# Optimization experiments

Hardware: AMD Instinct MI355X
Metric: run time of the kernel (lower is better)

Reference implementation:

```python
import jax, jax.numpy as jnp
import numpy as np

B, C, T, DIN, DOUT = 8, 8, 256, 1536, 512
RADIUS = int(round(0.05 * T))  # radius = round(0.05 * Nframe)
NEG_INF = float(jnp.finfo(jnp.float32).min)


def _suppress_1d(scores):
    # Greedy temporal NMS along T for a single cine. scores: [T]
    order = jnp.argsort(-scores)  # descending
    pos = jnp.arange(T)

    def step(carry, i):
        mask, s = carry
        keep = mask[i]
        window = (jnp.abs(pos - i) <= RADIUS) & (pos != i)
        mask = jnp.where(keep, mask & ~window, mask)
        s = jnp.where(keep, s, s.at[i].set(NEG_INF))
        return (mask, s), None

    (_, s), _ = jax.lax.scan(step, (jnp.ones(T, dtype=bool), scores), order)
    return s


def _top_p_mask(scores, p):
    # scores: [B, Tflat] non-negative; returns float {0,1} mask (detached).
    s = jax.lax.stop_gradient(scores)
    s = jnp.maximum(jnp.where(jnp.isfinite(s), s, 0.0), 0.0)
    sorted_idx = jnp.argsort(-s, axis=-1)
    sorted_s = jnp.take_along_axis(s, sorted_idx, axis=-1)
    norm = sorted_s / (sorted_s.sum(axis=-1, keepdims=True) + 1e-8)
    cum = jnp.cumsum(norm, axis=-1)
    keep = cum <= p
    keep = keep.at[..., :3].set(True)  # always keep top-3
    b_idx = jnp.arange(s.shape[0])[:, None]
    mask = jnp.zeros_like(s, dtype=bool).at[b_idx, sorted_idx].set(keep)
    return mask.astype(scores.dtype)


def setup_inputs() -> dict:
    key = jax.random.key(0)
    ks = jax.random.split(key, 6)
    return {
        "query": jax.random.normal(ks[0], (B, C, T, DIN), dtype=jnp.float32),
        "values": jax.random.normal(ks[1], (B, C, T, DIN), dtype=jnp.float32),
        "W1_w": jax.random.normal(ks[2], (DIN, DOUT), dtype=jnp.float32) / np.sqrt(DIN),
        "W1_b": jax.random.normal(ks[3], (DOUT,), dtype=jnp.float32) * 0.01,
        "V_w": jax.random.normal(ks[4], (DOUT, 1), dtype=jnp.float32) / np.sqrt(DOUT),
        "V_b": jax.random.normal(ks[5], (1,), dtype=jnp.float32) * 0.01,
    }


def reference(query, values, W1_w, W1_b, V_w, V_b):
    # raw_before_suppression = V(tanh(W1(query)))  -> [B, C, T, 1]
    h = jnp.tanh(jnp.einsum('bctd,de->bcte', query, W1_w) + W1_b)
    raw_before = jnp.einsum('bcte,eo->bcto', h, V_w) + V_b

    # greedy temporal suppression, vmapped over B*C cines
    flat = raw_before[..., 0].reshape(B * C, T)
    raw = jax.vmap(_suppress_1d)(flat).reshape(B, C, T, 1)

    score = jax.nn.sigmoid(raw)
    Tflat = C * T
    flat_probs = score[..., 0].reshape(B, Tflat)
    flat_probs = jnp.where(jnp.isfinite(flat_probs), flat_probs, 0.0)

    # eval path: top_p = 0.7 nucleus mask (detached)
    mask = _top_p_mask(flat_probs, 0.7)
    mask = (mask > 0).astype(flat_probs.dtype)

    masked_score = (flat_probs * mask).reshape(B, C, T, 1)
    sum_score = jnp.sum(masked_score, axis=(1, 2), keepdims=True)
    attn = masked_score / (sum_score + 1e-8)
    attn = jnp.where(sum_score <= 0, jnp.full_like(attn, 1.0 / Tflat), attn)

    context = jnp.sum(attn * values, axis=(1, 2))  # [B, DIN]
    return context, attn, masked_score
```

## Files before the change

kernel.cpp:

```cpp
#include <hip/hip_runtime.h>
#include <math.h>
#include <stdint.h>

#define TM 16384
#define NN 512
#define KDIM 1536
#define BM 128
#define BN 128
#define BKS 32
#define NKT 48

typedef _Float16 f16x8 __attribute__((ext_vector_type(8)));
typedef float f32x4 __attribute__((ext_vector_type(4)));

__device__ __forceinline__ unsigned short f16bits(_Float16 h) {
  union { _Float16 h; unsigned short u; } cv; cv.h = h; return cv.u;
}

__device__ __forceinline__ int swz_chunk(int row, int chunk) {
  return chunk ^ ((row >> 1) & 3);
}

__device__ __forceinline__ void gload_lds16(const void* g, void* l) {
  __builtin_amdgcn_global_load_lds(
      (const __attribute__((address_space(1))) unsigned int*)g,
      (__attribute__((address_space(3))) unsigned int*)l, 16, 0, 0);
}

__global__ __launch_bounds__(256) void convert_w1_kernel(
    const float* __restrict__ W1,
    unsigned short* __restrict__ W1ws)
{
  const int kt = blockIdx.x;
  const int nb = blockIdx.y;
  const int tid = threadIdx.x;
  const int k0 = kt * BKS, n0 = nb * BN;
  const size_t tbase = ((size_t)(nb * NKT + kt) * 2) * 4096;
#pragma unroll
  for (int i = 0; i < 16; ++i) {
    int idx = tid + i * 256;
    int nn = idx & 127, kk = idx >> 7;
    float f = W1[(size_t)(k0 + kk) * NN + n0 + nn];
    _Float16 h = (_Float16)f;
    _Float16 l = (_Float16)((f - (float)h) * 2048.0f);
    int off16 = nn * 32 + (swz_chunk(nn, kk >> 3) << 3) + (kk & 7);
    W1ws[tbase + off16] = f16bits(h);
    W1ws[tbase + 4096 + off16] = f16bits(l);
  }
}

__global__ __launch_bounds__(256, 2) void gemm_score_kernel(
    const float* __restrict__ query,
    const unsigned short* __restrict__ W1ws,
    const float* __restrict__ W1b,
    const float* __restrict__ Vw,
    float* __restrict__ raw_part)
{
  __shared__ __align__(16) char ldsb[2][32768];
  __shared__ float red[2][BM];

  const int tid = threadIdx.x;
  const int lane = tid & 63;
  const int w = tid >> 6;
  const int wr = w >> 1, wc = w & 1;
  const int lrow = lane & 15;
  const int lseg = lane >> 4;

  const int bid = blockIdx.x;
  const int lin = (bid & 7) * 64 + (bid >> 3);
  const int mb = lin >> 2, nb = lin & 3;
  const int m0 = mb * BM, n0 = nb * BN;

  f32x4 zero = {0.f, 0.f, 0.f, 0.f};
  f32x4 acc[4][4];
  f32x4 acc2[4][4];
#pragma unroll
  for (int m = 0; m < 4; ++m)
#pragma unroll
    for (int n = 0; n < 4; ++n) { acc[m][n] = zero; acc2[m][n] = zero; }

  const char* wbase = (const char*)W1ws;

  auto STAGE = [&](int kt, int bufi) {
    char* base = &ldsb[bufi][0];
    const int k0 = kt * BKS;
#pragma unroll
    for (int j = 0; j < 4; ++j) {
      int chunk = (w * 4 + j) * 64 + lane;
      int row = chunk >> 3, cp = chunk & 7;
      int kc = cp ^ (row & 7);
      gload_lds16(query + (size_t)(m0 + row) * KDIM + k0 + kc * 4,
                  base + (w * 4 + j) * 1024);
    }
    const char* tb = wbase + ((size_t)(nb * NKT + kt) * 2) * 8192;
#pragma unroll
    for (int j = 0; j < 2; ++j) {
      int off = w * 2048 + j * 1024;
      gload_lds16(tb + off + lane * 16, base + 16384 + off);
      gload_lds16(tb + 8192 + off + lane * 16, base + 24576 + off);
    }
  };

  STAGE(0, 0);
  for (int kt = 0; kt < NKT; ++kt) {
    const int cur = kt & 1;
    if (kt + 1 < NKT) {
      STAGE(kt + 1, cur ^ 1);
      asm volatile("s_waitcnt vmcnt(8)" ::: "memory");
    } else {
      asm volatile("s_waitcnt vmcnt(0)" ::: "memory");
    }
    __builtin_amdgcn_s_barrier();

    const char* base = &ldsb[cur][0];
    f16x8 afh[4], afl[4], bfh[4], bfl[4];
#pragma unroll
    for (int m = 0; m < 4; ++m) {
      int row = wr * 64 + m * 16 + lrow;
      int c0 = (lseg * 2) ^ (row & 7);
      int c1 = (lseg * 2 + 1) ^ (row & 7);
      f32x4 va = *reinterpret_cast<const f32x4*>(base + row * 128 + c0 * 16);
      f32x4 vb = *reinterpret_cast<const f32x4*>(base + row * 128 + c1 * 16);
      f16x8 h, l;
#pragma unroll
      for (int e = 0; e < 4; ++e) {
        _Float16 hh = (_Float16)va[e];
        h[e] = hh;
        l[e] = (_Float16)((va[e] - (float)hh) * 2048.0f);
      }
#pragma unroll
      for (int e = 0; e < 4; ++e) {
        _Float16 hh = (_Float16)vb[e];
        h[4 + e] = hh;
        l[4 + e] = (_Float16)((vb[e] - (float)hh) * 2048.0f);
      }
      afh[m] = h;
      afl[m] = l;
    }
#pragma unroll
    for (int n = 0; n < 4; ++n) {
      int row = wc * 64 + n * 16 + lrow;
      int off = row * 64 + (swz_chunk(row, lseg) << 4);
      bfh[n] = *reinterpret_cast<const f16x8*>(base + 16384 + off);
      bfl[n] = *reinterpret_cast<const f16x8*>(base + 24576 + off);
    }
#pragma unroll
    for (int m = 0; m < 4; ++m)
#pragma unroll
      for (int n = 0; n < 4; ++n) {
        acc[m][n]  = __builtin_amdgcn_mfma_f32_16x16x32_f16(afh[m], bfh[n], acc[m][n], 0, 0, 0);
        acc2[m][n] = __builtin_amdgcn_mfma_f32_16x16x32_f16(afh[m], bfl[n], acc2[m][n], 0, 0, 0);
        acc2[m][n] = __builtin_amdgcn_mfma_f32_16x16x32_f16(afl[m], bfh[n], acc2[m][n], 0, 0, 0);
      }
    asm volatile("s_waitcnt lgkmcnt(0)" ::: "memory");
    __builtin_amdgcn_s_barrier();
  }

  float part[4][4];
#pragma unroll
  for (int m = 0; m < 4; ++m)
#pragma unroll
    for (int r = 0; r < 4; ++r) part[m][r] = 0.f;
#pragma unroll
  for (int n = 0; n < 4; ++n) {
    int col = n0 + wc * 64 + n * 16 + lrow;
    float bias = W1b[col];
    float vw = Vw[col];
#pragma unroll
    for (int m = 0; m < 4; ++m)
#pragma unroll
      for (int r = 0; r < 4; ++r) {
        float z = acc[m][n][r] + acc2[m][n][r] * 4.8828125e-4f + bias;
        part[m][r] += tanhf(z) * vw;
      }
  }
#pragma unroll
  for (int off = 1; off < 16; off <<= 1)
#pragma unroll
    for (int m = 0; m < 4; ++m)
#pragma unroll
      for (int r = 0; r < 4; ++r)
        part[m][r] += __shfl_xor(part[m][r], off, 64);
  if (lrow == 0) {
#pragma unroll
    for (int m = 0; m < 4; ++m)
#pragma unroll
      for (int r = 0; r < 4; ++r)
        red[wc][wr * 64 + m * 16 + (lane >> 4) * 4 + r] = part[m][r];
  }
  __syncthreads();
  if (tid < BM)
    raw_part[(size_t)nb * TM + m0 + tid] = red[0][tid] + red[1][tid];
}

__global__ __launch_bounds__(64) void nms_kernel(
    const float* __restrict__ raw_part,
    const float* __restrict__ Vb,
    float* __restrict__ probs)
{
  const int cine = blockIdx.x;
  const int lane = threadIdx.x;
  __shared__ float s[256];
  __shared__ int order[256];
  float sv[4];
  const float vb = Vb[0];
#pragma unroll
  for (int q = 0; q < 4; ++q) {
    int p = q * 64 + lane;
    int idx = cine * 256 + p;
    float r = vb;
#pragma unroll
    for (int sl = 0; sl < 4; ++sl) r += raw_part[sl * TM + idx];
    sv[q] = r;
    s[p] = r;
  }
  __syncthreads();
#pragma unroll
  for (int q = 0; q < 4; ++q) {
    int p = q * 64 + lane;
    float st = sv[q];
    int rk = 0;
    for (int j = 0; j < 256; ++j) {
      float sj = s[j];
      rk += (sj > st) || (sj == st && j < p);
    }
    order[rk] = p;
  }
  __syncthreads();
  unsigned m = 0xFu;
  for (int r = 0; r < 256; ++r) {
    int i = order[r];
    int qi = i >> 6, li = i & 63;
    unsigned long long ball = __ballot((lane == li) && ((m >> qi) & 1u));
    if (ball) {
#pragma unroll
      for (int q = 0; q < 4; ++q) {
        int d = q * 64 + lane - i;
        if (d != 0 && d <= 13 && d >= -13) m &= ~(1u << q);
      }
    } else if (lane == li) {
      s[i] = -3.402823466385289e+38f;
    }
  }
  __syncthreads();
#pragma unroll
  for (int q = 0; q < 4; ++q) {
    int p = q * 64 + lane;
    probs[cine * 256 + p] = 1.0f / (1.0f + expf(-s[p]));
  }
}

__global__ __launch_bounds__(256) void topp_kernel(
    const float* __restrict__ probs,
    float* __restrict__ out)
{
  const int b = blockIdx.x;
  const int tid = threadIdx.x;
  __shared__ float p[2048];
  __shared__ int cnz[2048];
  __shared__ float sv[2048];
  __shared__ int sidx[2048];
  __shared__ unsigned char msk[2048];
  __shared__ float red[256];
  __shared__ int nnz_s;

  if (tid == 0) nnz_s = 0;
  for (int i = tid; i < 2048; i += 256) {
    p[i] = probs[b * 2048 + i];
    msk[i] = 0;
  }
  __syncthreads();
  float lsum = 0.f;
  for (int i = tid; i < 2048; i += 256) {
    float v = p[i];
    lsum += v;
    if (v > 0.f) {
      int slot = atomicAdd(&nnz_s, 1);
      cnz[slot] = i;
    }
  }
  red[tid] = lsum;
  __syncthreads();
  for (int sred = 128; sred > 0; sred >>= 1) {
    if (tid < sred) red[tid] += red[tid + sred];
    __syncthreads();
  }
  const int nnz = nnz_s;
  const float total = red[0];
  for (int c = tid; c < nnz; c += 256) {
    int i = cnz[c];
    float pi = p[i];
    int rank = 0;
    for (int cc = 0; cc < nnz; ++cc) {
      int j = cnz[cc];
      float pj = p[j];
      rank += (pj > pi) || (pj == pi && j < i);
    }
    sv[rank] = pi;
    sidx[rank] = i;
  }
  __syncthreads();
  if (tid == 0) {
    float denom = total + 1e-8f;
    float cum = 0.f;
    for (int r = 0; r < nnz; ++r) {
      cum += sv[r] / denom;
      if ((cum <= 0.7f) || (r < 3)) msk[sidx[r]] = 1;
    }
  }
  __syncthreads();
  float ls = 0.f;
  for (int i = tid; i < 2048; i += 256) {
    float m = msk[i] ? p[i] : 0.f;
    sv[i] = m;
    ls += m;
  }
  red[tid] = ls;
  __syncthreads();
  for (int sred = 128; sred > 0; sred >>= 1) {
    if (tid < sred) red[tid] += red[tid + sred];
    __syncthreads();
  }
  const float ssum = red[0];
  const float denom = ssum + 1e-8f;
  const bool uni = (ssum <= 0.f);
  for (int i = tid; i < 2048; i += 256) {
    float m = sv[i];
    out[28672 + b * 2048 + i] = m;
    out[12288 + b * 2048 + i] = uni ? (1.0f / 2048.0f) : (m / denom);
  }
}

__global__ __launch_bounds__(256) void ctx_part_kernel(
    const float* __restrict__ attn,
    const float* __restrict__ values,
    float* __restrict__ ctxp)
{
  const int ch = blockIdx.x % 6;
  const int g  = (blockIdx.x / 6) & 7;
  const int b  = blockIdx.x / 48;
  const int tid = threadIdx.x;
  const int lane = tid & 63, w = tid >> 6;
  __shared__ float av[256];
  __shared__ int   idx[256];
  __shared__ int   wcnt[4];

  float a = attn[b * 2048 + g * 256 + tid];
  unsigned long long mask = __ballot(a != 0.f);
  if (lane == 0) wcnt[w] = __popcll(mask);
  __syncthreads();
  int base = 0;
  for (int i = 0; i < w; ++i) base += wcnt[i];
  if (a != 0.f) {
    int pos = base + __popcll(mask & ((1ull << lane) - 1ull));
    av[pos] = a;
    idx[pos] = g * 256 + tid;
  }
  __syncthreads();
  const int total = wcnt[0] + wcnt[1] + wcnt[2] + wcnt[3];
  const int d = ch * 256 + tid;
  float acc = 0.f;
#pragma unroll 4
  for (int t = 0; t < total; ++t)
    acc += av[t] * values[((size_t)b * 2048 + idx[t]) * KDIM + d];
  ctxp[((size_t)(b * 8 + g)) * KDIM + d] = acc;
}

__global__ __launch_bounds__(256) void ctx_reduce_kernel(
    const float* __restrict__ ctxp,
    float* __restrict__ out)
{
  const int i = blockIdx.x * 256 + threadIdx.x;
  const int b = i / KDIM, d = i % KDIM;
  float sum = 0.f;
#pragma unroll
  for (int g = 0; g < 8; ++g) sum += ctxp[((size_t)(b * 8 + g)) * KDIM + d];
  out[i] = sum;
}

extern "C" void kernel_launch(void* const* d_in, const int* in_sizes, int n_in,
                              void* d_out, int out_size, void* d_ws, size_t ws_size,
                              hipStream_t stream) {
  const float* query  = (const float*)d_in[0];
  const float* values = (const float*)d_in[1];
  const float* W1w    = (const float*)d_in[2];
  const float* W1b    = (const float*)d_in[3];
  const float* Vw     = (const float*)d_in[4];
  const float* Vb     = (const float*)d_in[5];
  float* out = (float*)d_out;

  unsigned short* W1ws = (unsigned short*)d_ws;
  float* raw_part = (float*)((char*)d_ws + 3145728);
  float* probs    = raw_part + 4 * TM;
  float* ctxp     = probs + TM;

  convert_w1_kernel<<<dim3(NKT, 4), 256, 0, stream>>>(W1w, W1ws);
  gemm_score_kernel<<<512, 256, 0, stream>>>(query, W1ws, W1b, Vw, raw_part);
  nms_kernel<<<64, 64, 0, stream>>>(raw_part, Vb, probs);
  topp_kernel<<<8, 256, 0, stream>>>(probs, out);
  ctx_part_kernel<<<384, 256, 0, stream>>>(out + 12288, values, ctxp);
  ctx_reduce_kernel<<<48, 256, 0, stream>>>(ctxp, out);
}
```

Before: 171.2 us.

## Use 8-wave GEMM blocks and fuse NMS with top-p into one kernel

The GEMM block grows from 4 to 8 waves, each computing a 32x64 sub-tile instead of 64x64. This shrinks per-wave accumulators and raises occupancy for better latency hiding, at the cost of fewer MFMAs per LDS fragment load. The NMS and top-p kernels are merged into one 512-thread block per batch, with each wave handling one cine's suppression. This removes a launch and the round trip of the probs buffer through global memory, but NMS now runs on only 8 blocks instead of 64.

```diff
diff --git a/kernel.cpp b/kernel.cpp
--- a/kernel.cpp
+++ b/kernel.cpp
@@ -49,7 +49,7 @@
   }
 }
 
-__global__ __launch_bounds__(256, 2) void gemm_score_kernel(
+__global__ __launch_bounds__(512, 4) void gemm_score_kernel(
     const float* __restrict__ query,
     const unsigned short* __restrict__ W1ws,
     const float* __restrict__ W1b,
@@ -62,7 +62,7 @@
   const int tid = threadIdx.x;
   const int lane = tid & 63;
   const int w = tid >> 6;
-  const int wr = w >> 1, wc = w & 1;
+  const int wr = w & 3, wc = w >> 2;
   const int lrow = lane & 15;
   const int lseg = lane >> 4;
 
@@ -72,10 +72,10 @@
   const int m0 = mb * BM, n0 = nb * BN;
 
   f32x4 zero = {0.f, 0.f, 0.f, 0.f};
-  f32x4 acc[4][4];
-  f32x4 acc2[4][4];
-#pragma unroll
-  for (int m = 0; m < 4; ++m)
+  f32x4 acc[2][4];
+  f32x4 acc2[2][4];
+#pragma unroll
+  for (int m = 0; m < 2; ++m)
 #pragma unroll
     for (int n = 0; n < 4; ++n) { acc[m][n] = zero; acc2[m][n] = zero; }
 
@@ -85,20 +85,16 @@
     char* base = &ldsb[bufi][0];
     const int k0 = kt * BKS;
 #pragma unroll
-    for (int j = 0; j < 4; ++j) {
-      int chunk = (w * 4 + j) * 64 + lane;
+    for (int j = 0; j < 2; ++j) {
+      int chunk = (w * 2 + j) * 64 + lane;
       int row = chunk >> 3, cp = chunk & 7;
       int kc = cp ^ (row & 7);
       gload_lds16(query + (size_t)(m0 + row) * KDIM + k0 + kc * 4,
-                  base + (w * 4 + j) * 1024);
+                  base + (w * 2 + j) * 1024);
     }
     const char* tb = wbase + ((size_t)(nb * NKT + kt) * 2) * 8192;
-#pragma unroll
-    for (int j = 0; j < 2; ++j) {
-      int off = w * 2048 + j * 1024;
-      gload_lds16(tb + off + lane * 16, base + 16384 + off);
-      gload_lds16(tb + 8192 + off + lane * 16, base + 24576 + off);
-    }
+    gload_lds16(tb + w * 1024 + lane * 16, base + 16384 + w * 1024);
+    gload_lds16(tb + 8192 + w * 1024 + lane * 16, base + 24576 + w * 1024);
   };
 
   STAGE(0, 0);
@@ -106,17 +102,17 @@
     const int cur = kt & 1;
     if (kt + 1 < NKT) {
       STAGE(kt + 1, cur ^ 1);
-      asm volatile("s_waitcnt vmcnt(8)" ::: "memory");
+      asm volatile("s_waitcnt vmcnt(4)" ::: "memory");
     } else {
       asm volatile("s_waitcnt vmcnt(0)" ::: "memory");
     }
     __builtin_amdgcn_s_barrier();
 
     const char* base = &ldsb[cur][0];
-    f16x8 afh[4], afl[4], bfh[4], bfl[4];
-#pragma unroll
-    for (int m = 0; m < 4; ++m) {
-      int row = wr * 64 + m * 16 + lrow;
+    f16x8 afh[2], afl[2], bfh[4], bfl[4];
+#pragma unroll
+    for (int m = 0; m < 2; ++m) {
+      int row = wr * 32 + m * 16 + lrow;
       int c0 = (lseg * 2) ^ (row & 7);
       int c1 = (lseg * 2 + 1) ^ (row & 7);
       f32x4 va = *reinterpret_cast<const f32x4*>(base + row * 128 + c0 * 16);
@@ -145,7 +141,7 @@
       bfl[n] = *reinterpret_cast<const f16x8*>(base + 24576 + off);
     }
 #pragma unroll
-    for (int m = 0; m < 4; ++m)
+    for (int m = 0; m < 2; ++m)
 #pragma unroll
       for (int n = 0; n < 4; ++n) {
         acc[m][n]  = __builtin_amdgcn_mfma_f32_16x16x32_f16(afh[m], bfh[n], acc[m][n], 0, 0, 0);
@@ -156,9 +152,9 @@
     __builtin_amdgcn_s_barrier();
   }
 
-  float part[4][4];
-#pragma unroll
-  for (int m = 0; m < 4; ++m)
+  float part[2][4];
+#pragma unroll
+  for (int m = 0; m < 2; ++m)
 #pragma unroll
     for (int r = 0; r < 4; ++r) part[m][r] = 0.f;
 #pragma unroll
@@ -167,7 +163,7 @@
     float bias = W1b[col];
     float vw = Vw[col];
 #pragma unroll
-    for (int m = 0; m < 4; ++m)
+    for (int m = 0; m < 2; ++m)
 #pragma unroll
       for (int r = 0; r < 4; ++r) {
         float z = acc[m][n][r] + acc2[m][n][r] * 4.8828125e-4f + bias;
@@ -177,32 +173,42 @@
 #pragma unroll
   for (int off = 1; off < 16; off <<= 1)
 #pragma unroll
-    for (int m = 0; m < 4; ++m)
+    for (int m = 0; m < 2; ++m)
 #pragma unroll
       for (int r = 0; r < 4; ++r)
         part[m][r] += __shfl_xor(part[m][r], off, 64);
   if (lrow == 0) {
 #pragma unroll
-    for (int m = 0; m < 4; ++m)
+    for (int m = 0; m < 2; ++m)
 #pragma unroll
       for (int r = 0; r < 4; ++r)
-        red[wc][wr * 64 + m * 16 + (lane >> 4) * 4 + r] = part[m][r];
+        red[wc][wr * 32 + m * 16 + (lane >> 4) * 4 + r] = part[m][r];
   }
   __syncthreads();
   if (tid < BM)
     raw_part[(size_t)nb * TM + m0 + tid] = red[0][tid] + red[1][tid];
 }
 
-__global__ __launch_bounds__(64) void nms_kernel(
+__global__ __launch_bounds__(512) void nms_topp_kernel(
     const float* __restrict__ raw_part,
     const float* __restrict__ Vb,
-    float* __restrict__ probs)
-{
-  const int cine = blockIdx.x;
-  const int lane = threadIdx.x;
-  __shared__ float s[256];
-  __shared__ int order[256];
-  float sv[4];
+    float* __restrict__ out)
+{
+  const int b = blockIdx.x;
+  const int tid = threadIdx.x;
+  const int lane = tid & 63;
+  const int w = tid >> 6;
+  const int cine = b * 8 + w;
+
+  __shared__ float s[8][256];
+  __shared__ int order[8][256];
+  __shared__ float sv[2048];
+  __shared__ int sidx[2048];
+  __shared__ unsigned char msk[2048];
+  __shared__ float red[512];
+  __shared__ int nnz_s;
+
+  float pv[4];
   const float vb = Vb[0];
 #pragma unroll
   for (int q = 0; q < 4; ++q) {
@@ -211,25 +217,25 @@
     float r = vb;
 #pragma unroll
     for (int sl = 0; sl < 4; ++sl) r += raw_part[sl * TM + idx];
-    sv[q] = r;
-    s[p] = r;
+    pv[q] = r;
+    s[w][p] = r;
   }
   __syncthreads();
 #pragma unroll
   for (int q = 0; q < 4; ++q) {
     int p = q * 64 + lane;
-    float st = sv[q];
+    float st = pv[q];
     int rk = 0;
     for (int j = 0; j < 256; ++j) {
-      float sj = s[j];
+      float sj = s[w][j];
       rk += (sj > st) || (sj == st && j < p);
     }
-    order[rk] = p;
+    order[w][rk] = p;
   }
   __syncthreads();
   unsigned m = 0xFu;
   for (int r = 0; r < 256; ++r) {
-    int i = order[r];
+    int i = order[w][r];
     int qi = i >> 6, li = i & 63;
     unsigned long long ball = __ballot((lane == li) && ((m >> qi) & 1u));
     if (ball) {
@@ -239,39 +245,24 @@
         if (d != 0 && d <= 13 && d >= -13) m &= ~(1u << q);
       }
     } else if (lane == li) {
-      s[i] = -3.402823466385289e+38f;
-    }
-  }
-  __syncthreads();
+      s[w][i] = -3.402823466385289e+38f;
+    }
+  }
+  __syncthreads();
+  float* p = &s[0][0];
+  int* cnz = &order[0][0];
+  if (tid == 0) nnz_s = 0;
 #pragma unroll
   for (int q = 0; q < 4; ++q) {
-    int p = q * 64 + lane;
-    probs[cine * 256 + p] = 1.0f / (1.0f + expf(-s[p]));
-  }
-}
-
-__global__ __launch_bounds__(256) void topp_kernel(
-    const float* __restrict__ probs,
-    float* __restrict__ out)
-{
-  const int b = blockIdx.x;
-  const int tid = threadIdx.x;
-  __shared__ float p[2048];
-  __shared__ int cnz[2048];
-  __shared__ float sv[2048];
-  __shared__ int sidx[2048];
-  __shared__ unsigned char msk[2048];
-  __shared__ float red[256];
-  __shared__ int nnz_s;
-
-  if (tid == 0) nnz_s = 0;
-  for (int i = tid; i < 2048; i += 256) {
-    p[i] = probs[b * 2048 + i];
-    msk[i] = 0;
+    int pos = q * 64 + lane;
+    s[w][pos] = 1.0f / (1.0f + expf(-s[w][pos]));
+    msk[w * 256 + pos] = 0;
   }
   __syncthreads();
   float lsum = 0.f;
-  for (int i = tid; i < 2048; i += 256) {
+#pragma unroll
+  for (int i0 = 0; i0 < 4; ++i0) {
+    int i = tid + i0 * 512;
     float v = p[i];
     lsum += v;
     if (v > 0.f) {
@@ -281,13 +272,13 @@
   }
   red[tid] = lsum;
   __syncthreads();
-  for (int sred = 128; sred > 0; sred >>= 1) {
+  for (int sred = 256; sred > 0; sred >>= 1) {
     if (tid < sred) red[tid] += red[tid + sred];
     __syncthreads();
   }
   const int nnz = nnz_s;
   const float total = red[0];
-  for (int c = tid; c < nnz; c += 256) {
+  for (int c = tid; c < nnz; c += 512) {
     int i = cnz[c];
     float pi = p[i];
     int rank = 0;
@@ -310,24 +301,28 @@
   }
   __syncthreads();
   float ls = 0.f;
-  for (int i = tid; i < 2048; i += 256) {
-    float m = msk[i] ? p[i] : 0.f;
-    sv[i] = m;
-    ls += m;
+#pragma unroll
+  for (int i0 = 0; i0 < 4; ++i0) {
+    int i = tid + i0 * 512;
+    float mm = msk[i] ? p[i] : 0.f;
+    sv[i] = mm;
+    ls += mm;
   }
   red[tid] = ls;
   __syncthreads();
-  for (int sred = 128; sred > 0; sred >>= 1) {
+  for (int sred = 256; sred > 0; sred >>= 1) {
     if (tid < sred) red[tid] += red[tid + sred];
     __syncthreads();
   }
   const float ssum = red[0];
   const float denom = ssum + 1e-8f;
   const bool uni = (ssum <= 0.f);
-  for (int i = tid; i < 2048; i += 256) {
-    float m = sv[i];
-    out[28672 + b * 2048 + i] = m;
-    out[12288 + b * 2048 + i] = uni ? (1.0f / 2048.0f) : (m / denom);
+#pragma unroll
+  for (int i0 = 0; i0 < 4; ++i0) {
+    int i = tid + i0 * 512;
+    float mm = sv[i];
+    out[28672 + b * 2048 + i] = mm;
+    out[12288 + b * 2048 + i] = uni ? (1.0f / 2048.0f) : (mm / denom);
   }
 }
 
@@ -391,13 +386,11 @@
 
   unsigned short* W1ws = (unsigned short*)d_ws;
   float* raw_part = (float*)((char*)d_ws + 3145728);
-  float* probs    = raw_part + 4 * TM;
-  float* ctxp     = probs + TM;
+  float* ctxp     = raw_part + 4 * TM;
 
   convert_w1_kernel<<<dim3(NKT, 4), 256, 0, stream>>>(W1w, W1ws);
-  gemm_score_kernel<<<512, 256, 0, stream>>>(query, W1ws, W1b, Vw, raw_part);
-  nms_kernel<<<64, 64, 0, stream>>>(raw_part, Vb, probs);
-  topp_kernel<<<8, 256, 0, stream>>>(probs, out);
+  gemm_score_kernel<<<512, 512, 0, stream>>>(query, W1ws, W1b, Vw, raw_part);
+  nms_topp_kernel<<<8, 512, 0, stream>>>(raw_part, Vb, out);
   ctx_part_kernel<<<384, 256, 0, stream>>>(out + 12288, values, ctxp);
   ctx_reduce_kernel<<<48, 256, 0, stream>>>(ctxp, out);
 }
```

New measurement: 173.2 us. Within noise of the previous version (+1.2%).

## Split GEMM tile across eight waves with one M-fragment each

Applied to the files above, without the earlier changes.

The score GEMM block grows from 4 to 8 waves. Each wave now owns a 16-row strip across all 128 columns instead of a 64x64 quadrant, so the cross-wave LDS reduction disappears and each wave writes its own rows. The fp32-to-fp16 split conversion switches to packed cvt_pkrtz, which rounds toward zero rather than to nearest; the low-part residual still captures the difference. The trade-off is lower register pressure and more waves for latency hiding, against every wave re-reading all B fragments from LDS, which raises LDS traffic per MFMA.

```diff
diff --git a/kernel.cpp b/kernel.cpp
--- a/kernel.cpp
+++ b/kernel.cpp
@@ -11,6 +11,7 @@
 #define NKT 48
 
 typedef _Float16 f16x8 __attribute__((ext_vector_type(8)));
+typedef __fp16 h16x2 __attribute__((ext_vector_type(2)));
 typedef float f32x4 __attribute__((ext_vector_type(4)));
 
 __device__ __forceinline__ unsigned short f16bits(_Float16 h) {
@@ -49,7 +50,7 @@
   }
 }
 
-__global__ __launch_bounds__(256, 2) void gemm_score_kernel(
+__global__ __launch_bounds__(512, 4) void gemm_score_kernel(
     const float* __restrict__ query,
     const unsigned short* __restrict__ W1ws,
     const float* __restrict__ W1b,
@@ -57,12 +58,10 @@
     float* __restrict__ raw_part)
 {
   __shared__ __align__(16) char ldsb[2][32768];
-  __shared__ float red[2][BM];
 
   const int tid = threadIdx.x;
   const int lane = tid & 63;
   const int w = tid >> 6;
-  const int wr = w >> 1, wc = w & 1;
   const int lrow = lane & 15;
   const int lseg = lane >> 4;
 
@@ -72,12 +71,9 @@
   const int m0 = mb * BM, n0 = nb * BN;
 
   f32x4 zero = {0.f, 0.f, 0.f, 0.f};
-  f32x4 acc[4][4];
-  f32x4 acc2[4][4];
-#pragma unroll
-  for (int m = 0; m < 4; ++m)
-#pragma unroll
-    for (int n = 0; n < 4; ++n) { acc[m][n] = zero; acc2[m][n] = zero; }
+  f32x4 acc[8], acc2[8];
+#pragma unroll
+  for (int n = 0; n < 8; ++n) { acc[n] = zero; acc2[n] = zero; }
 
   const char* wbase = (const char*)W1ws;
 
@@ -85,20 +81,16 @@
     char* base = &ldsb[bufi][0];
     const int k0 = kt * BKS;
 #pragma unroll
-    for (int j = 0; j < 4; ++j) {
-      int chunk = (w * 4 + j) * 64 + lane;
+    for (int j = 0; j < 2; ++j) {
+      int chunk = (w * 2 + j) * 64 + lane;
       int row = chunk >> 3, cp = chunk & 7;
       int kc = cp ^ (row & 7);
       gload_lds16(query + (size_t)(m0 + row) * KDIM + k0 + kc * 4,
-                  base + (w * 4 + j) * 1024);
+                  base + (w * 2 + j) * 1024);
     }
     const char* tb = wbase + ((size_t)(nb * NKT + kt) * 2) * 8192;
-#pragma unroll
-    for (int j = 0; j < 2; ++j) {
-      int off = w * 2048 + j * 1024;
-      gload_lds16(tb + off + lane * 16, base + 16384 + off);
-      gload_lds16(tb + 8192 + off + lane * 16, base + 24576 + off);
-    }
+    gload_lds16(tb + w * 1024 + lane * 16, base + 16384 + w * 1024);
+    gload_lds16(tb + 8192 + w * 1024 + lane * 16, base + 24576 + w * 1024);
   };
 
   STAGE(0, 0);
@@ -106,91 +98,77 @@
     const int cur = kt & 1;
     if (kt + 1 < NKT) {
       STAGE(kt + 1, cur ^ 1);
-      asm volatile("s_waitcnt vmcnt(8)" ::: "memory");
+      asm volatile("s_waitcnt vmcnt(4)" ::: "memory");
     } else {
       asm volatile("s_waitcnt vmcnt(0)" ::: "memory");
     }
     __builtin_amdgcn_s_barrier();
 
     const char* base = &ldsb[cur][0];
-    f16x8 afh[4], afl[4], bfh[4], bfl[4];
-#pragma unroll
-    for (int m = 0; m < 4; ++m) {
-      int row = wr * 64 + m * 16 + lrow;
+    f16x8 afh, afl;
+    {
+      int row = w * 16 + lrow;
       int c0 = (lseg * 2) ^ (row & 7);
       int c1 = (lseg * 2 + 1) ^ (row & 7);
       f32x4 va = *reinterpret_cast<const f32x4*>(base + row * 128 + c0 * 16);
       f32x4 vb = *reinterpret_cast<const f32x4*>(base + row * 128 + c1 * 16);
-      f16x8 h, l;
-#pragma unroll
-      for (int e = 0; e < 4; ++e) {
-        _Float16 hh = (_Float16)va[e];
-        h[e] = hh;
-        l[e] = (_Float16)((va[e] - (float)hh) * 2048.0f);
-      }
-#pragma unroll
-      for (int e = 0; e < 4; ++e) {
-        _Float16 hh = (_Float16)vb[e];
-        h[4 + e] = hh;
-        l[4 + e] = (_Float16)((vb[e] - (float)hh) * 2048.0f);
-      }
-      afh[m] = h;
-      afl[m] = l;
-    }
-#pragma unroll
-    for (int n = 0; n < 4; ++n) {
-      int row = wc * 64 + n * 16 + lrow;
-      int off = row * 64 + (swz_chunk(row, lseg) << 4);
-      bfh[n] = *reinterpret_cast<const f16x8*>(base + 16384 + off);
-      bfl[n] = *reinterpret_cast<const f16x8*>(base + 24576 + off);
-    }
-#pragma unroll
-    for (int m = 0; m < 4; ++m)
-#pragma unroll
-      for (int n = 0; n < 4; ++n) {
-        acc[m][n]  = __builtin_amdgcn_mfma_f32_16x16x32_f16(afh[m], bfh[n], acc[m][n], 0, 0, 0);
-        acc2[m][n] = __builtin_amdgcn_mfma_f32_16x16x32_f16(afh[m], bfl[n], acc2[m][n], 0, 0, 0);
-        acc2[m][n] = __builtin_amdgcn_mfma_f32_16x16x32_f16(afl[m], bfh[n], acc2[m][n], 0, 0, 0);
-      }
+      union H8 { f16x8 v; h16x2 p[4]; } h, l;
+      h.p[0] = __builtin_amdgcn_cvt_pkrtz(va[0], va[1]);
+      h.p[1] = __builtin_amdgcn_cvt_pkrtz(va[2], va[3]);
+      h.p[2] = __builtin_amdgcn_cvt_pkrtz(vb[0], vb[1]);
+      h.p[3] = __builtin_amdgcn_cvt_pkrtz(vb[2], vb[3]);
+      float r0 = (va[0] - (float)h.p[0][0]) * 2048.0f;
+      float r1 = (va[1] - (float)h.p[0][1]) * 2048.0f;
+      float r2 = (va[2] - (float)h.p[1][0]) * 2048.0f;
+      float r3 = (va[3] - (float)h.p[1][1]) * 2048.0f;
+      float r4 = (vb[0] - (float)h.p[2][0]) * 2048.0f;
+      float r5 = (vb[1] - (float)h.p[2][1]) * 2048.0f;
+      float r6 = (vb[2] - (float)h.p[3][0]) * 2048.0f;
+      float r7 = (vb[3] - (float)h.p[3][1]) * 2048.0f;
+      l.p[0] = __builtin_amdgcn_cvt_pkrtz(r0, r1);
+      l.p[1] = __builtin_amdgcn_cvt_pkrtz(r2, r3);
+      l.p[2] = __builtin_amdgcn_cvt_pkrtz(r4, r5);
+      l.p[3] = __builtin_amdgcn_cvt_pkrtz(r6, r7);
+      afh = h.v;
+      afl = l.v;
+    }
+#pragma unroll
+    for (int nf = 0; nf < 8; ++nf) {
+      int brow = nf * 16 + lrow;
+      int boff = brow * 64 + (swz_chunk(brow, lseg) << 4);
+      f16x8 bh = *reinterpret_cast<const f16x8*>(base + 16384 + boff);
+      f16x8 bl = *reinterpret_cast<const f16x8*>(base + 24576 + boff);
+      acc[nf]  = __builtin_amdgcn_mfma_f32_16x16x32_f16(afh, bh, acc[nf], 0, 0, 0);
+      acc2[nf] = __builtin_amdgcn_mfma_f32_16x16x32_f16(afh, bl, acc2[nf], 0, 0, 0);
+      acc2[nf] = __builtin_amdgcn_mfma_f32_16x16x32_f16(afl, bh, acc2[nf], 0, 0, 0);
+    }
     asm volatile("s_waitcnt lgkmcnt(0)" ::: "memory");
     __builtin_amdgcn_s_barrier();
   }
 
-  float part[4][4];
-#pragma unroll
-  for (int m = 0; m < 4; ++m)
-#pragma unroll
-    for (int r = 0; r < 4; ++r) part[m][r] = 0.f;
-#pragma unroll
-  for (int n = 0; n < 4; ++n) {
-    int col = n0 + wc * 64 + n * 16 + lrow;
+  float part[4] = {0.f, 0.f, 0.f, 0.f};
+#pragma unroll
+  for (int nf = 0; nf < 8; ++nf) {
+    int col = n0 + nf * 16 + lrow;
     float bias = W1b[col];
     float vw = Vw[col];
 #pragma unroll
-    for (int m = 0; m < 4; ++m)
-#pragma unroll
-      for (int r = 0; r < 4; ++r) {
-        float z = acc[m][n][r] + acc2[m][n][r] * 4.8828125e-4f + bias;
-        part[m][r] += tanhf(z) * vw;
-      }
+    for (int r = 0; r < 4; ++r) {
+      float z = acc[nf][r] + acc2[nf][r] * 4.8828125e-4f + bias;
+      part[r] += tanhf(z) * vw;
+    }
   }
 #pragma unroll
   for (int off = 1; off < 16; off <<= 1)
 #pragma unroll
-    for (int m = 0; m < 4; ++m)
-#pragma unroll
-      for (int r = 0; r < 4; ++r)
-        part[m][r] += __shfl_xor(part[m][r], off, 64);
+    for (int r = 0; r < 4; ++r)
+      part[r] += __shfl_xor(part[r], off, 64);
   if (lrow == 0) {
-#pragma unroll
-    for (int m = 0; m < 4; ++m)
-#pragma unroll
-      for (int r = 0; r < 4; ++r)
-        red[wc][wr * 64 + m * 16 + (lane >> 4) * 4 + r] = part[m][r];
-  }
-  __syncthreads();
-  if (tid < BM)
-    raw_part[(size_t)nb * TM + m0 + tid] = red[0][tid] + red[1][tid];
+    int rowb = m0 + w * 16 + lseg * 4;
+#pragma unroll
+    for (int r = 0; r < 4; ++r)
+      raw_part[(size_t)nb * TM + rowb + r] = part[r];
+  }
 }
 
 __global__ __launch_bounds__(64) void nms_kernel(
@@ -395,7 +373,7 @@
   float* ctxp     = probs + TM;
 
   convert_w1_kernel<<<dim3(NKT, 4), 256, 0, stream>>>(W1w, W1ws);
-  gemm_score_kernel<<<512, 256, 0, stream>>>(query, W1ws, W1b, Vw, raw_part);
+  gemm_score_kernel<<<512, 512, 0, stream>>>(query, W1ws, W1b, Vw, raw_part);
   nms_kernel<<<64, 64, 0, stream>>>(raw_part, Vb, probs);
   topp_kernel<<<8, 256, 0, stream>>>(probs, out);
   ctx_part_kernel<<<384, 256, 0, stream>>>(out + 12288, values, ctxp);
```

Result: faster. 166.8 us (-2.6%).
